# Kernel optimization log

Measured on AMD Instinct MI355X. Metric: run time of the kernel, lower is better.

Reference implementation:

```python
import jax, jax.numpy as jnp
import numpy as np

D = 1024
H = 4
HD = D // H
B = 256
L = 64
DILATIONS = (1, 4, 8, 16)


def setup_inputs() -> dict:
    key = jax.random.key(0)
    ks = jax.random.split(key, 12)
    s = 1.0 / np.sqrt(D)
    return {
        "x": jax.random.normal(ks[0], (B, D), jnp.float32),
        "hist": jax.random.normal(ks[1], (L, B, D), jnp.float32),
        "Wq": jax.random.normal(ks[2], (D, D), jnp.float32) * s,
        "bq": jnp.zeros((D,), jnp.float32),
        "Wk": jax.random.normal(ks[3], (D, D), jnp.float32) * s,
        "bk": jnp.zeros((D,), jnp.float32),
        "Wv": jax.random.normal(ks[4], (D, D), jnp.float32) * s,
        "bv": jnp.zeros((D,), jnp.float32),
        "Wo": jax.random.normal(ks[5], (D, D), jnp.float32) * s,
        "bo": jnp.zeros((D,), jnp.float32),
        "dil_w": jnp.full((len(DILATIONS),), 1.0 / len(DILATIONS), jnp.float32),
        "gamma": jnp.ones((D,), jnp.float32),
        "beta": jnp.zeros((D,), jnp.float32),
    }


def reference(x, hist, Wq, bq, Wk, bk, Wv, bv, Wo, bo, dil_w, gamma, beta):
    scale = 1.0 / np.sqrt(HD)
    q = (x @ Wq + bq).reshape(B, H, HD)  # (B, H, HD)
    attended = []
    for d in DILATIONS:
        # history frames at stride d, concatenated along dim 0 (faithful to torch.cat)
        frames = hist[::d].reshape(-1, D)              # (T', D), T' = ceil(L/d)*B
        k = (frames @ Wk + bk).reshape(-1, H, HD)      # (T', H, HD)
        v = (frames @ Wv + bv).reshape(-1, H, HD)
        s = jnp.einsum('bhd,thd->bht', q, k) * scale   # (B, H, T')
        a = jax.nn.softmax(s, axis=-1)
        attended.append(jnp.einsum('bht,thd->bhd', a, v).reshape(B, D))
    w = jax.nn.softmax(dil_w, axis=0)
    combined = sum(w[i] * attended[i] for i in range(len(DILATIONS)))
    y = x + combined @ Wo + bo
    mu = jnp.mean(y, axis=-1, keepdims=True)
    var = jnp.var(y, axis=-1, keepdims=True)
    return (y - mu) / jnp.sqrt(var + 1e-5) * gamma + beta
```

## Files before the change

### kernel.cpp

```cpp
#include <hip/hip_runtime.h>


#define DD    1024
#define TALL  16384

typedef _Float16 half8  __attribute__((ext_vector_type(8)));
typedef _Float16 half4v __attribute__((ext_vector_type(4)));
typedef float    floatx4 __attribute__((ext_vector_type(4)));
typedef unsigned int u32;

static const size_t OFF_WQT = 0;
static const size_t OFF_WKT = 2097152;
static const size_t OFF_WVT = 4194304;
static const size_t OFF_WOT = 6291456;
static const size_t OFF_XB  = 8388608;
static const size_t OFF_QS  = 8912896;
static const size_t OFF_HB  = 16777216;
static const size_t OFF_S   = OFF_HB;
static const size_t OFF_KB  = 50331648;
static const size_t OFF_PVP = OFF_KB;
static const size_t OFF_VT  = 83886080;
static const size_t OFF_OPP = 117440512;
static const size_t OFF_CB  = 134483968;

__device__ __forceinline__ void gl_lds16(const void* g, void* l) {
  __builtin_amdgcn_global_load_lds((const __attribute__((address_space(1))) u32*)g,
                                   (__attribute__((address_space(3))) u32*)l, 16, 0, 0);
}

__global__ void wtrans_kernel(const float* __restrict__ W0, const float* __restrict__ W1,
                              const float* __restrict__ W2, const float* __restrict__ W3,
                              _Float16* __restrict__ T0, _Float16* __restrict__ T1,
                              _Float16* __restrict__ T2, _Float16* __restrict__ T3) {
  const float* W; _Float16* T;
  switch (blockIdx.z) {
    case 0: W = W0; T = T0; break;
    case 1: W = W1; T = T1; break;
    case 2: W = W2; T = T2; break;
    default: W = W3; T = T3; break;
  }
  __shared__ float tile[32][33];
  int tx = threadIdx.x & 31, ty = threadIdx.x >> 5;
  int k0 = blockIdx.x * 32, n0 = blockIdx.y * 32;
#pragma unroll
  for (int i = 0; i < 4; i++) {
    int r = ty + i * 8;
    tile[r][tx] = W[(size_t)(k0 + r) * DD + n0 + tx];
  }
  __syncthreads();
#pragma unroll
  for (int i = 0; i < 4; i++) {
    int r = ty + i * 8;
    T[(size_t)(n0 + r) * DD + k0 + tx] = (_Float16)tile[tx][r];
  }
}

__global__ void cvt2_kernel(const float* __restrict__ a, _Float16* __restrict__ oa, int na4,
                            const float* __restrict__ b, _Float16* __restrict__ ob, int nb4) {
  int i = blockIdx.x * 256 + threadIdx.x;
  const float* src; _Float16* dst;
  if (i < na4) { src = a; dst = oa; }
  else { i -= na4; if (i >= nb4) return; src = b; dst = ob; }
  float4 v = ((const float4*)src)[i];
  half4v h = {(_Float16)v.x, (_Float16)v.y, (_Float16)v.z, (_Float16)v.w};
  *(half4v*)(dst + 4 * (size_t)i) = h;
}

__device__ __forceinline__ void gemm_core(const _Float16* __restrict__ A, size_t lda,
                                          const _Float16* __restrict__ B, size_t ldb,
                                          int kIters, _Float16* As, _Float16* Bs,
                                          int tid, floatx4 acc[4][4]) {
  int lane = tid & 63, w = tid >> 6;
  int l15 = lane & 15, quad = lane >> 4;
  int wm = (w >> 1) * 64, wn = (w & 1) * 64;
  int swz = ((tid & 3) ^ ((tid >> 3) & 3)) * 8;
  int pch = (quad ^ ((l15 >> 1) & 3)) * 8;
  const char* gA0 = (const char*)(A + (size_t)(tid >> 2) * lda + swz);
  const char* gA1 = (const char*)(A + ((size_t)(tid >> 2) + 64) * lda + swz);
  const char* gB0 = (const char*)(B + (size_t)(tid >> 2) * ldb + swz);
  const char* gB1 = (const char*)(B + ((size_t)(tid >> 2) + 64) * ldb + swz);
  _Float16* lA0 = As + w * 512; _Float16* lA1 = As + 2048 + w * 512;
  _Float16* lB0 = Bs + w * 512; _Float16* lB1 = Bs + 2048 + w * 512;
  for (int kk = 0; kk < kIters; kk++) {
    __syncthreads();
    size_t off = (size_t)kk * 64;
    gl_lds16(gA0 + off, lA0);
    gl_lds16(gA1 + off, lA1);
    gl_lds16(gB0 + off, lB0);
    gl_lds16(gB1 + off, lB1);
    __syncthreads();
    half8 a[4];
#pragma unroll
    for (int mi = 0; mi < 4; mi++) a[mi] = *(const half8*)&As[(wm + mi * 16 + l15) * 32 + pch];
#pragma unroll
    for (int ni = 0; ni < 4; ni++) {
      half8 b8 = *(const half8*)&Bs[(wn + ni * 16 + l15) * 32 + pch];
#pragma unroll
      for (int mi = 0; mi < 4; mi++)
        acc[mi][ni] = __builtin_amdgcn_mfma_f32_16x16x32_f16(a[mi], b8, acc[mi][ni], 0, 0, 0);
    }
  }
}

template <bool OUTF32>
__launch_bounds__(256, 3)
__global__ void gemm_f16_kernel(const _Float16* __restrict__ A, size_t lda, size_t aoffz,
                                const _Float16* __restrict__ B, size_t ldb, size_t boffz,
                                int kIters, const float* __restrict__ bias, float scale,
                                void* __restrict__ C, size_t ldc, size_t coffz) {
  __shared__ __align__(16) _Float16 As[4096];
  __shared__ __align__(16) _Float16 Bs[4096];
  int tid = threadIdx.x;
  const _Float16* Ab = A + aoffz * blockIdx.z + (size_t)(blockIdx.y * 128) * lda;
  const _Float16* Bb = B + boffz * blockIdx.z + (size_t)(blockIdx.x * 128) * ldb;
  floatx4 acc[4][4];
  floatx4 zero = {0.f, 0.f, 0.f, 0.f};
#pragma unroll
  for (int a = 0; a < 4; a++)
#pragma unroll
    for (int b = 0; b < 4; b++) acc[a][b] = zero;
  gemm_core(Ab, lda, Bb, ldb, kIters, As, Bs, tid, acc);
  int lane = tid & 63, w = tid >> 6;
  int l15 = lane & 15, quad = lane >> 4;
  int wm = (w >> 1) * 64, wn = (w & 1) * 64;
#pragma unroll
  for (int mi = 0; mi < 4; mi++)
#pragma unroll
    for (int ni = 0; ni < 4; ni++) {
      int colg = blockIdx.x * 128 + wn + ni * 16 + l15;
      float bv = bias ? bias[colg] : 0.f;
#pragma unroll
      for (int r = 0; r < 4; r++) {
        int rowg = blockIdx.y * 128 + wm + mi * 16 + quad * 4 + r;
        float v = (acc[mi][ni][r] + bv) * scale;
        size_t idx = coffz * blockIdx.z + (size_t)rowg * ldc + colg;
        if (OUTF32) ((float*)C)[idx] = v;
        else ((_Float16*)C)[idx] = (_Float16)v;
      }
    }
}

__launch_bounds__(256, 2)
__global__ void gemm_kv_kernel(const _Float16* __restrict__ A,
                               const _Float16* __restrict__ WkT, const _Float16* __restrict__ WvT,
                               const float* __restrict__ bk, const float* __restrict__ bv,
                               _Float16* __restrict__ K, _Float16* __restrict__ Vt) {
  __shared__ __align__(16) _Float16 As[4096];
  __shared__ __align__(16) _Float16 Bk[4096];
  __shared__ __align__(16) _Float16 Bv[4096];
  int tid = threadIdx.x;
  int lane = tid & 63, w = tid >> 6;
  int l15 = lane & 15, quad = lane >> 4;
  int wm = (w >> 1) * 64, wn = (w & 1) * 64;
  int m0 = blockIdx.y * 128, n0 = blockIdx.x * 128;
  int swz = ((tid & 3) ^ ((tid >> 3) & 3)) * 8;
  int pch = (quad ^ ((l15 >> 1) & 3)) * 8;
  floatx4 accK[4][4], accV[4][4];
  floatx4 zero = {0.f, 0.f, 0.f, 0.f};
#pragma unroll
  for (int a = 0; a < 4; a++)
#pragma unroll
    for (int b = 0; b < 4; b++) { accK[a][b] = zero; accV[a][b] = zero; }
  const char* gA0 = (const char*)(A + ((size_t)m0 + (tid >> 2)) * 1024 + swz);
  const char* gA1 = gA0 + 64 * 1024 * 2;
  const char* gK0 = (const char*)(WkT + ((size_t)n0 + (tid >> 2)) * 1024 + swz);
  const char* gK1 = gK0 + 64 * 1024 * 2;
  const char* gV0 = (const char*)(WvT + ((size_t)n0 + (tid >> 2)) * 1024 + swz);
  const char* gV1 = gV0 + 64 * 1024 * 2;
  _Float16* lA0 = As + w * 512; _Float16* lA1 = As + 2048 + w * 512;
  _Float16* lK0 = Bk + w * 512; _Float16* lK1 = Bk + 2048 + w * 512;
  _Float16* lV0 = Bv + w * 512; _Float16* lV1 = Bv + 2048 + w * 512;
  for (int kk = 0; kk < 32; kk++) {
    __syncthreads();
    size_t off = (size_t)kk * 64;
    gl_lds16(gA0 + off, lA0); gl_lds16(gA1 + off, lA1);
    gl_lds16(gK0 + off, lK0); gl_lds16(gK1 + off, lK1);
    gl_lds16(gV0 + off, lV0); gl_lds16(gV1 + off, lV1);
    __syncthreads();
    half8 a[4];
#pragma unroll
    for (int mi = 0; mi < 4; mi++) a[mi] = *(const half8*)&As[(wm + mi * 16 + l15) * 32 + pch];
#pragma unroll
    for (int ni = 0; ni < 4; ni++) {
      half8 k8 = *(const half8*)&Bk[(wn + ni * 16 + l15) * 32 + pch];
      half8 v8 = *(const half8*)&Bv[(wn + ni * 16 + l15) * 32 + pch];
#pragma unroll
      for (int mi = 0; mi < 4; mi++) {
        accK[mi][ni] = __builtin_amdgcn_mfma_f32_16x16x32_f16(a[mi], k8, accK[mi][ni], 0, 0, 0);
        accV[mi][ni] = __builtin_amdgcn_mfma_f32_16x16x32_f16(a[mi], v8, accV[mi][ni], 0, 0, 0);
      }
    }
  }
#pragma unroll
  for (int mi = 0; mi < 4; mi++)
#pragma unroll
    for (int ni = 0; ni < 4; ni++) {
      int col = n0 + wn + ni * 16 + l15;
      float bkv = bk[col], bvv = bv[col];
      int row0 = m0 + wm + mi * 16 + quad * 4;
#pragma unroll
      for (int r = 0; r < 4; r++)
        K[(size_t)(row0 + r) * 1024 + col] = (_Float16)(accK[mi][ni][r] + bkv);
      half4v vv = {(_Float16)(accV[mi][ni][0] + bvv), (_Float16)(accV[mi][ni][1] + bvv),
                   (_Float16)(accV[mi][ni][2] + bvv), (_Float16)(accV[mi][ni][3] + bvv)};
      *(half4v*)&Vt[(size_t)col * TALL + row0] = vv;
    }
}

__global__ void softmax_kernel(_Float16* __restrict__ S, const float* __restrict__ dil_w) {
  int r = blockIdx.x, tid = threadIdx.x;
  _Float16* row = S + (size_t)r * TALL;
  int lane = tid & 63, w = tid >> 6;
  half8 v[8];
  float mloc = -1e30f;
#pragma unroll
  for (int i = 0; i < 8; i++) {
    v[i] = *(const half8*)&row[((size_t)i * 256 + tid) * 8];
#pragma unroll
    for (int j = 0; j < 8; j++) mloc = fmaxf(mloc, (float)v[i][j]);
  }
  __shared__ float wmax[4];
  __shared__ float Zf[64];
  __shared__ float Zd[4];
  __shared__ float cf[64];
#pragma unroll
  for (int off = 1; off <= 32; off <<= 1) mloc = fmaxf(mloc, __shfl_xor(mloc, off, 64));
  if (lane == 0) wmax[w] = mloc;
  __syncthreads();
  float m = fmaxf(fmaxf(wmax[0], wmax[1]), fmaxf(wmax[2], wmax[3]));
  float es[8];
#pragma unroll
  for (int i = 0; i < 8; i++) {
    float s = 0.f;
#pragma unroll
    for (int j = 0; j < 8; j++) s += __expf((float)v[i][j] - m);
#pragma unroll
    for (int off = 1; off <= 16; off <<= 1) s += __shfl_xor(s, off, 64);
    es[i] = s;
  }
  if ((lane & 31) == 0) {
    int half = tid >> 5;
#pragma unroll
    for (int i = 0; i < 8; i++) Zf[i * 8 + half] = es[i];
  }
  __syncthreads();
  if (tid < 4) {
    int step = 1 << (tid + (tid ? 1 : 0));
    float z = 0.f;
    for (int f = 0; f < 64; f += step) z += Zf[f];
    Zd[tid] = z;
  }
  __syncthreads();
  if (tid < 64) {
    float w0 = dil_w[0], w1 = dil_w[1], w2 = dil_w[2], w3 = dil_w[3];
    float wmx = fmaxf(fmaxf(w0, w1), fmaxf(w2, w3));
    float e0 = __expf(w0 - wmx), e1 = __expf(w1 - wmx), e2 = __expf(w2 - wmx), e3 = __expf(w3 - wmx);
    float wsum = e0 + e1 + e2 + e3;
    float c = (e0 / wsum) / Zd[0];
    if ((tid & 3) == 0) c += (e1 / wsum) / Zd[1];
    if ((tid & 7) == 0) c += (e2 / wsum) / Zd[2];
    if ((tid & 15) == 0) c += (e3 / wsum) / Zd[3];
    cf[tid] = c * 256.0f;
  }
  __syncthreads();
#pragma unroll
  for (int i = 0; i < 8; i++) {
    float c = cf[i * 8 + (tid >> 5)];
    half8 o;
#pragma unroll
    for (int j = 0; j < 8; j++) o[j] = (_Float16)(__expf((float)v[i][j] - m) * c);
    *(half8*)&row[((size_t)i * 256 + tid) * 8] = o;
  }
}

__launch_bounds__(256, 3)
__global__ void gemm_pv_kernel(const _Float16* __restrict__ P, const _Float16* __restrict__ Vt,
                               float* __restrict__ part) {
  __shared__ __align__(16) _Float16 As[4096];
  __shared__ __align__(16) _Float16 Bs[4096];
  int tid = threadIdx.x;
  int h = blockIdx.z >> 5, sp = blockIdx.z & 31;
  const _Float16* Ab = P + (size_t)h * 4194304 + (size_t)(blockIdx.y * 128) * TALL + sp * 512;
  const _Float16* Bb = Vt + (size_t)(h * 256 + blockIdx.x * 128) * TALL + sp * 512;
  floatx4 acc[4][4];
  floatx4 zero = {0.f, 0.f, 0.f, 0.f};
#pragma unroll
  for (int a = 0; a < 4; a++)
#pragma unroll
    for (int b = 0; b < 4; b++) acc[a][b] = zero;
  gemm_core(Ab, TALL, Bb, TALL, 16, As, Bs, tid, acc);
  int lane = tid & 63, w = tid >> 6;
  int l15 = lane & 15, quad = lane >> 4;
  int wm = (w >> 1) * 64, wn = (w & 1) * 64;
#pragma unroll
  for (int mi = 0; mi < 4; mi++)
#pragma unroll
    for (int ni = 0; ni < 4; ni++) {
      int featg = h * 256 + blockIdx.x * 128 + wn + ni * 16 + l15;
#pragma unroll
      for (int r = 0; r < 4; r++) {
        int q = blockIdx.y * 128 + wm + mi * 16 + quad * 4 + r;
        part[((size_t)(sp * 256 + q)) * 1024 + featg] = acc[mi][ni][r];
      }
    }
}

__global__ void reduce_kernel(const float* __restrict__ part, _Float16* __restrict__ comb) {
  int q = blockIdx.x;
  int f4 = threadIdx.x * 4;
  float4 s = {0.f, 0.f, 0.f, 0.f};
  for (int sp = 0; sp < 32; sp++) {
    float4 p = *(const float4*)&part[((size_t)(sp * 256 + q)) * 1024 + f4];
    s.x += p.x; s.y += p.y; s.z += p.z; s.w += p.w;
  }
  const float inv = 1.f / 256.f;
  half4v o = {(_Float16)(s.x * inv), (_Float16)(s.y * inv), (_Float16)(s.z * inv), (_Float16)(s.w * inv)};
  *(half4v*)&comb[(size_t)q * 1024 + f4] = o;
}

__global__ void ln_kernel(const float* __restrict__ x, const float* __restrict__ part2,
                          const float* __restrict__ bo, const float* __restrict__ gamma,
                          const float* __restrict__ beta, float* __restrict__ out) {
  int b = blockIdx.x, t = threadIdx.x;
  __shared__ float red[8];
  float y[4];
  float sum = 0.f, sq = 0.f;
#pragma unroll
  for (int i = 0; i < 4; i++) {
    int j = t + i * 256;
    float v = x[(size_t)b * 1024 + j] + bo[j];
#pragma unroll
    for (int z = 0; z < 4; z++) v += part2[(size_t)z * 262144 + (size_t)b * 1024 + j];
    y[i] = v;
    sum += v;
    sq += v * v;
  }
#pragma unroll
  for (int off = 1; off < 64; off <<= 1) {
    sum += __shfl_xor(sum, off, 64);
    sq += __shfl_xor(sq, off, 64);
  }
  int w = t >> 6, lane = t & 63;
  if (lane == 0) { red[w] = sum; red[4 + w] = sq; }
  __syncthreads();
  sum = red[0] + red[1] + red[2] + red[3];
  sq = red[4] + red[5] + red[6] + red[7];
  float mu = sum * (1.f / 1024.f);
  float var = sq * (1.f / 1024.f) - mu * mu;
  float inv = rsqrtf(var + 1e-5f);
#pragma unroll
  for (int i = 0; i < 4; i++) {
    int j = t + i * 256;
    out[(size_t)b * 1024 + j] = (y[i] - mu) * inv * gamma[j] + beta[j];
  }
}

extern "C" void kernel_launch(void* const* d_in, const int* in_sizes, int n_in,
                              void* d_out, int out_size, void* d_ws, size_t ws_size,
                              hipStream_t stream) {
  const float* x     = (const float*)d_in[0];
  const float* hist  = (const float*)d_in[1];
  const float* Wq    = (const float*)d_in[2];
  const float* bq    = (const float*)d_in[3];
  const float* Wk    = (const float*)d_in[4];
  const float* bk    = (const float*)d_in[5];
  const float* Wv    = (const float*)d_in[6];
  const float* bv    = (const float*)d_in[7];
  const float* Wo    = (const float*)d_in[8];
  const float* bo    = (const float*)d_in[9];
  const float* dil_w = (const float*)d_in[10];
  const float* gamma = (const float*)d_in[11];
  const float* beta  = (const float*)d_in[12];
  char* ws = (char*)d_ws;

  _Float16* WqT   = (_Float16*)(ws + OFF_WQT);
  _Float16* WkT   = (_Float16*)(ws + OFF_WKT);
  _Float16* WvT   = (_Float16*)(ws + OFF_WVT);
  _Float16* WoT   = (_Float16*)(ws + OFF_WOT);
  _Float16* xb    = (_Float16*)(ws + OFF_XB);
  _Float16* Qs    = (_Float16*)(ws + OFF_QS);
  _Float16* histb = (_Float16*)(ws + OFF_HB);
  _Float16* Sb    = (_Float16*)(ws + OFF_S);
  _Float16* Kb    = (_Float16*)(ws + OFF_KB);
  _Float16* Vtb   = (_Float16*)(ws + OFF_VT);
  float* pvpart   = (float*)(ws + OFF_PVP);
  float* oppart   = (float*)(ws + OFF_OPP);
  _Float16* comb  = (_Float16*)(ws + OFF_CB);

  wtrans_kernel<<<dim3(32, 32, 4), 256, 0, stream>>>(Wq, Wk, Wv, Wo, WqT, WkT, WvT, WoT);
  cvt2_kernel<<<dim3(16640), 256, 0, stream>>>(hist, histb, 4194304, x, xb, 65536);
  gemm_f16_kernel<false><<<dim3(8, 2, 1), 256, 0, stream>>>(
      xb, 1024, 0, WqT, 1024, 0, 32, bq, 0.0625f, (void*)Qs, 1024, 0);
  gemm_kv_kernel<<<dim3(8, 128), 256, 0, stream>>>(histb, WkT, WvT, bk, bv, Kb, Vtb);
  gemm_f16_kernel<false><<<dim3(128, 2, 4), 256, 0, stream>>>(
      Qs, 1024, 256, Kb, 1024, 256, 8, nullptr, 1.0f, (void*)Sb, TALL, 4194304);
  softmax_kernel<<<dim3(1024), 256, 0, stream>>>(Sb, dil_w);
  gemm_pv_kernel<<<dim3(2, 2, 128), 256, 0, stream>>>(Sb, Vtb, pvpart);
  reduce_kernel<<<dim3(256), 256, 0, stream>>>(pvpart, comb);
  gemm_f16_kernel<true><<<dim3(8, 2, 4), 256, 0, stream>>>(
      comb, 1024, 256, WoT, 1024, 256, 8, nullptr, 1.0f, (void*)oppart, 1024, 262144);
  ln_kernel<<<dim3(256), 256, 0, stream>>>(x, oppart, bo, gamma, beta, (float*)d_out);
}
```

Before: 327.4 us.

## Reassociate attention to avoid computing K and V projections over history

Rather than projecting all 16384 history frames through Wk and Wv, the query is folded into Wk per head (G = Q·Wk_h^T) so scores come straight from G·hist^T. Likewise P·hist is computed first, then multiplied by a precomputed fused Wv·Wo per head. The bv·Wo term is added in the layernorm kernel, and bk is dropped because it shifts every score in a row equally. This removes the large KV GEMM and its stores, but adds a transposed fp16 copy of hist, a P·hist GEMM with a 4096-wide per-head output, and a split-K partial reduction.

```diff
diff --git a/kernel.cpp b/kernel.cpp
--- a/kernel.cpp
+++ b/kernel.cpp
@@ -9,61 +9,94 @@
 typedef float    floatx4 __attribute__((ext_vector_type(4)));
 typedef unsigned int u32;
 
-static const size_t OFF_WQT = 0;
-static const size_t OFF_WKT = 2097152;
-static const size_t OFF_WVT = 4194304;
-static const size_t OFF_WOT = 6291456;
-static const size_t OFF_XB  = 8388608;
-static const size_t OFF_QS  = 8912896;
-static const size_t OFF_HB  = 16777216;
-static const size_t OFF_S   = OFF_HB;
-static const size_t OFF_KB  = 50331648;
-static const size_t OFF_PVP = OFF_KB;
-static const size_t OFF_VT  = 83886080;
-static const size_t OFF_OPP = 117440512;
-static const size_t OFF_CB  = 134483968;
+static const size_t OFF_WQT  = 0;
+static const size_t OFF_WOT  = 2097152;
+static const size_t OFF_WV16 = 4194304;
+static const size_t OFF_WK16 = 6291456;
+static const size_t OFF_XB   = 8388608;
+static const size_t OFF_QS   = 8912896;
+static const size_t OFF_G    = 9437184;
+static const size_t OFF_WVOT = 11534336;
+static const size_t OFF_BVWO = 19922944;
+static const size_t OFF_OPP  = 19988480;
+static const size_t OFF_PHR  = 24182784;
+static const size_t OFF_HB   = 33554432;
+static const size_t OFF_PHP  = OFF_HB;
+static const size_t OFF_HT   = 67108864;
+static const size_t OFF_S    = 100663296;
 
 __device__ __forceinline__ void gl_lds16(const void* g, void* l) {
   __builtin_amdgcn_global_load_lds((const __attribute__((address_space(1))) u32*)g,
                                    (__attribute__((address_space(3))) u32*)l, 16, 0, 0);
 }
 
-__global__ void wtrans_kernel(const float* __restrict__ W0, const float* __restrict__ W1,
-                              const float* __restrict__ W2, const float* __restrict__ W3,
-                              _Float16* __restrict__ T0, _Float16* __restrict__ T1,
-                              _Float16* __restrict__ T2, _Float16* __restrict__ T3) {
-  const float* W; _Float16* T;
-  switch (blockIdx.z) {
-    case 0: W = W0; T = T0; break;
-    case 1: W = W1; T = T1; break;
-    case 2: W = W2; T = T2; break;
-    default: W = W3; T = T3; break;
-  }
-  __shared__ float tile[32][33];
-  int tx = threadIdx.x & 31, ty = threadIdx.x >> 5;
-  int k0 = blockIdx.x * 32, n0 = blockIdx.y * 32;
-#pragma unroll
-  for (int i = 0; i < 4; i++) {
-    int r = ty + i * 8;
-    tile[r][tx] = W[(size_t)(k0 + r) * DD + n0 + tx];
-  }
-  __syncthreads();
-#pragma unroll
-  for (int i = 0; i < 4; i++) {
-    int r = ty + i * 8;
-    T[(size_t)(n0 + r) * DD + k0 + tx] = (_Float16)tile[tx][r];
-  }
-}
-
-__global__ void cvt2_kernel(const float* __restrict__ a, _Float16* __restrict__ oa, int na4,
-                            const float* __restrict__ b, _Float16* __restrict__ ob, int nb4) {
-  int i = blockIdx.x * 256 + threadIdx.x;
-  const float* src; _Float16* dst;
-  if (i < na4) { src = a; dst = oa; }
-  else { i -= na4; if (i >= nb4) return; src = b; dst = ob; }
-  float4 v = ((const float4*)src)[i];
-  half4v h = {(_Float16)v.x, (_Float16)v.y, (_Float16)v.z, (_Float16)v.w};
-  *(half4v*)(dst + 4 * (size_t)i) = h;
+__global__ void prep_kernel(const float* __restrict__ Wq, const float* __restrict__ Wo,
+                            const float* __restrict__ Wv, const float* __restrict__ Wk,
+                            const float* __restrict__ hist, const float* __restrict__ x,
+                            _Float16* __restrict__ WqT, _Float16* __restrict__ WoT,
+                            _Float16* __restrict__ Wv16, _Float16* __restrict__ Wk16,
+                            _Float16* __restrict__ histb, _Float16* __restrict__ histT,
+                            _Float16* __restrict__ xb) {
+  int bid = blockIdx.x, tid = threadIdx.x;
+  if (bid < 2048) {
+    const float* W = (bid < 1024) ? Wq : Wo;
+    _Float16* T = (bid < 1024) ? WqT : WoT;
+    int tile = bid & 1023;
+    int k0 = (tile & 31) * 32, n0 = (tile >> 5) * 32;
+    __shared__ float t32[32][33];
+    int tx = tid & 31, ty = tid >> 5;
+#pragma unroll
+    for (int i = 0; i < 4; i++) {
+      int r = ty + i * 8;
+      t32[r][tx] = W[(size_t)(k0 + r) * DD + n0 + tx];
+    }
+    __syncthreads();
+#pragma unroll
+    for (int i = 0; i < 4; i++) {
+      int r = ty + i * 8;
+      T[(size_t)(n0 + r) * DD + k0 + tx] = (_Float16)t32[tx][r];
+    }
+  } else if (bid < 20736) {
+    const float* src; _Float16* dst; size_t i;
+    if (bid < 3072)       { src = Wv;   dst = Wv16;  i = (size_t)(bid - 2048) * 256 + tid; }
+    else if (bid < 4096)  { src = Wk;   dst = Wk16;  i = (size_t)(bid - 3072) * 256 + tid; }
+    else if (bid < 20480) { src = hist; dst = histb; i = (size_t)(bid - 4096) * 256 + tid; }
+    else                  { src = x;    dst = xb;    i = (size_t)(bid - 20480) * 256 + tid; }
+    float4 v = ((const float4*)src)[i];
+    half4v h = {(_Float16)v.x, (_Float16)v.y, (_Float16)v.z, (_Float16)v.w};
+    *(half4v*)(dst + 4 * i) = h;
+  } else {
+    int tb = bid - 20736;
+    int t0 = (tb & 255) * 64, f0 = (tb >> 8) * 64;
+    __shared__ _Float16 lt[64][72];
+    int r = tid >> 2, c0 = (tid & 3) * 16;
+#pragma unroll
+    for (int i = 0; i < 4; i++) {
+      float4 v = *(const float4*)&hist[(size_t)(t0 + r) * 1024 + f0 + c0 + i * 4];
+      half4v h = {(_Float16)v.x, (_Float16)v.y, (_Float16)v.z, (_Float16)v.w};
+      *(half4v*)&lt[r][c0 + i * 4] = h;
+    }
+    __syncthreads();
+    int fr = tid >> 2, tc0 = (tid & 3) * 16;
+    half8 o0, o1;
+#pragma unroll
+    for (int j = 0; j < 8; j++) { o0[j] = lt[tc0 + j][fr]; o1[j] = lt[tc0 + 8 + j][fr]; }
+    *(half8*)&histT[(size_t)(f0 + fr) * TALL + t0 + tc0] = o0;
+    *(half8*)&histT[(size_t)(f0 + fr) * TALL + t0 + tc0 + 8] = o1;
+  }
+}
+
+__global__ void bvwo_kernel(const float* __restrict__ bv, const _Float16* __restrict__ WoT,
+                            float* __restrict__ bvwo) {
+  int j = blockIdx.x * 256 + threadIdx.x;
+  const half8* row = (const half8*)(WoT + (size_t)j * 1024);
+  float acc = 0.f;
+  for (int c = 0; c < 128; c++) {
+    half8 w = row[c];
+#pragma unroll
+    for (int e = 0; e < 8; e++) acc += bv[c * 8 + e] * (float)w[e];
+  }
+  bvwo[j] = acc;
 }
 
 __device__ __forceinline__ void gemm_core(const _Float16* __restrict__ A, size_t lda,
@@ -140,71 +173,51 @@
     }
 }
 
-__launch_bounds__(256, 2)
-__global__ void gemm_kv_kernel(const _Float16* __restrict__ A,
-                               const _Float16* __restrict__ WkT, const _Float16* __restrict__ WvT,
-                               const float* __restrict__ bk, const float* __restrict__ bv,
-                               _Float16* __restrict__ K, _Float16* __restrict__ Vt) {
+__launch_bounds__(256, 3)
+__global__ void gemm_ph_kernel(const _Float16* __restrict__ P, const _Float16* __restrict__ histT,
+                               float* __restrict__ part) {
   __shared__ __align__(16) _Float16 As[4096];
-  __shared__ __align__(16) _Float16 Bk[4096];
-  __shared__ __align__(16) _Float16 Bv[4096];
+  __shared__ __align__(16) _Float16 Bs[4096];
   int tid = threadIdx.x;
+  int h = blockIdx.z >> 3, sp = blockIdx.z & 7;
+  const _Float16* Ab = P + (size_t)h * 4194304 + (size_t)(blockIdx.y * 128) * TALL + sp * 2048;
+  const _Float16* Bb = histT + (size_t)(blockIdx.x * 128) * TALL + sp * 2048;
+  floatx4 acc[4][4];
+  floatx4 zero = {0.f, 0.f, 0.f, 0.f};
+#pragma unroll
+  for (int a = 0; a < 4; a++)
+#pragma unroll
+    for (int b = 0; b < 4; b++) acc[a][b] = zero;
+  gemm_core(Ab, TALL, Bb, TALL, 64, As, Bs, tid, acc);
   int lane = tid & 63, w = tid >> 6;
   int l15 = lane & 15, quad = lane >> 4;
   int wm = (w >> 1) * 64, wn = (w & 1) * 64;
-  int m0 = blockIdx.y * 128, n0 = blockIdx.x * 128;
-  int swz = ((tid & 3) ^ ((tid >> 3) & 3)) * 8;
-  int pch = (quad ^ ((l15 >> 1) & 3)) * 8;
-  floatx4 accK[4][4], accV[4][4];
-  floatx4 zero = {0.f, 0.f, 0.f, 0.f};
-#pragma unroll
-  for (int a = 0; a < 4; a++)
-#pragma unroll
-    for (int b = 0; b < 4; b++) { accK[a][b] = zero; accV[a][b] = zero; }
-  const char* gA0 = (const char*)(A + ((size_t)m0 + (tid >> 2)) * 1024 + swz);
-  const char* gA1 = gA0 + 64 * 1024 * 2;
-  const char* gK0 = (const char*)(WkT + ((size_t)n0 + (tid >> 2)) * 1024 + swz);
-  const char* gK1 = gK0 + 64 * 1024 * 2;
-  const char* gV0 = (const char*)(WvT + ((size_t)n0 + (tid >> 2)) * 1024 + swz);
-  const char* gV1 = gV0 + 64 * 1024 * 2;
-  _Float16* lA0 = As + w * 512; _Float16* lA1 = As + 2048 + w * 512;
-  _Float16* lK0 = Bk + w * 512; _Float16* lK1 = Bk + 2048 + w * 512;
-  _Float16* lV0 = Bv + w * 512; _Float16* lV1 = Bv + 2048 + w * 512;
-  for (int kk = 0; kk < 32; kk++) {
-    __syncthreads();
-    size_t off = (size_t)kk * 64;
-    gl_lds16(gA0 + off, lA0); gl_lds16(gA1 + off, lA1);
-    gl_lds16(gK0 + off, lK0); gl_lds16(gK1 + off, lK1);
-    gl_lds16(gV0 + off, lV0); gl_lds16(gV1 + off, lV1);
-    __syncthreads();
-    half8 a[4];
-#pragma unroll
-    for (int mi = 0; mi < 4; mi++) a[mi] = *(const half8*)&As[(wm + mi * 16 + l15) * 32 + pch];
+#pragma unroll
+  for (int mi = 0; mi < 4; mi++)
 #pragma unroll
     for (int ni = 0; ni < 4; ni++) {
-      half8 k8 = *(const half8*)&Bk[(wn + ni * 16 + l15) * 32 + pch];
-      half8 v8 = *(const half8*)&Bv[(wn + ni * 16 + l15) * 32 + pch];
-#pragma unroll
-      for (int mi = 0; mi < 4; mi++) {
-        accK[mi][ni] = __builtin_amdgcn_mfma_f32_16x16x32_f16(a[mi], k8, accK[mi][ni], 0, 0, 0);
-        accV[mi][ni] = __builtin_amdgcn_mfma_f32_16x16x32_f16(a[mi], v8, accV[mi][ni], 0, 0, 0);
+      int k = blockIdx.x * 128 + wn + ni * 16 + l15;
+#pragma unroll
+      for (int r = 0; r < 4; r++) {
+        int q = blockIdx.y * 128 + wm + mi * 16 + quad * 4 + r;
+        part[(size_t)blockIdx.z * 262144 + (size_t)q * 1024 + k] = acc[mi][ni][r];
       }
     }
-  }
-#pragma unroll
-  for (int mi = 0; mi < 4; mi++)
-#pragma unroll
-    for (int ni = 0; ni < 4; ni++) {
-      int col = n0 + wn + ni * 16 + l15;
-      float bkv = bk[col], bvv = bv[col];
-      int row0 = m0 + wm + mi * 16 + quad * 4;
-#pragma unroll
-      for (int r = 0; r < 4; r++)
-        K[(size_t)(row0 + r) * 1024 + col] = (_Float16)(accK[mi][ni][r] + bkv);
-      half4v vv = {(_Float16)(accV[mi][ni][0] + bvv), (_Float16)(accV[mi][ni][1] + bvv),
-                   (_Float16)(accV[mi][ni][2] + bvv), (_Float16)(accV[mi][ni][3] + bvv)};
-      *(half4v*)&Vt[(size_t)col * TALL + row0] = vv;
-    }
+}
+
+__global__ void reduce_ph_kernel(const float* __restrict__ part, _Float16* __restrict__ PHred) {
+  size_t e4 = ((size_t)blockIdx.x * 256 + threadIdx.x) * 4;
+  int q = (int)(e4 >> 12);
+  int hk = (int)(e4 & 4095);
+  int h = hk >> 10, k = hk & 1023;
+  float4 s = {0.f, 0.f, 0.f, 0.f};
+#pragma unroll
+  for (int sp = 0; sp < 8; sp++) {
+    float4 p = *(const float4*)&part[(size_t)(h * 8 + sp) * 262144 + (size_t)q * 1024 + k];
+    s.x += p.x; s.y += p.y; s.z += p.z; s.w += p.w;
+  }
+  half4v o = {(_Float16)s.x, (_Float16)s.y, (_Float16)s.z, (_Float16)s.w};
+  *(half4v*)&PHred[e4] = o;
 }
 
 __global__ void softmax_kernel(_Float16* __restrict__ S, const float* __restrict__ dil_w) {
@@ -273,54 +286,10 @@
   }
 }
 
-__launch_bounds__(256, 3)
-__global__ void gemm_pv_kernel(const _Float16* __restrict__ P, const _Float16* __restrict__ Vt,
-                               float* __restrict__ part) {
-  __shared__ __align__(16) _Float16 As[4096];
-  __shared__ __align__(16) _Float16 Bs[4096];
-  int tid = threadIdx.x;
-  int h = blockIdx.z >> 5, sp = blockIdx.z & 31;
-  const _Float16* Ab = P + (size_t)h * 4194304 + (size_t)(blockIdx.y * 128) * TALL + sp * 512;
-  const _Float16* Bb = Vt + (size_t)(h * 256 + blockIdx.x * 128) * TALL + sp * 512;
-  floatx4 acc[4][4];
-  floatx4 zero = {0.f, 0.f, 0.f, 0.f};
-#pragma unroll
-  for (int a = 0; a < 4; a++)
-#pragma unroll
-    for (int b = 0; b < 4; b++) acc[a][b] = zero;
-  gemm_core(Ab, TALL, Bb, TALL, 16, As, Bs, tid, acc);
-  int lane = tid & 63, w = tid >> 6;
-  int l15 = lane & 15, quad = lane >> 4;
-  int wm = (w >> 1) * 64, wn = (w & 1) * 64;
-#pragma unroll
-  for (int mi = 0; mi < 4; mi++)
-#pragma unroll
-    for (int ni = 0; ni < 4; ni++) {
-      int featg = h * 256 + blockIdx.x * 128 + wn + ni * 16 + l15;
-#pragma unroll
-      for (int r = 0; r < 4; r++) {
-        int q = blockIdx.y * 128 + wm + mi * 16 + quad * 4 + r;
-        part[((size_t)(sp * 256 + q)) * 1024 + featg] = acc[mi][ni][r];
-      }
-    }
-}
-
-__global__ void reduce_kernel(const float* __restrict__ part, _Float16* __restrict__ comb) {
-  int q = blockIdx.x;
-  int f4 = threadIdx.x * 4;
-  float4 s = {0.f, 0.f, 0.f, 0.f};
-  for (int sp = 0; sp < 32; sp++) {
-    float4 p = *(const float4*)&part[((size_t)(sp * 256 + q)) * 1024 + f4];
-    s.x += p.x; s.y += p.y; s.z += p.z; s.w += p.w;
-  }
-  const float inv = 1.f / 256.f;
-  half4v o = {(_Float16)(s.x * inv), (_Float16)(s.y * inv), (_Float16)(s.z * inv), (_Float16)(s.w * inv)};
-  *(half4v*)&comb[(size_t)q * 1024 + f4] = o;
-}
-
 __global__ void ln_kernel(const float* __restrict__ x, const float* __restrict__ part2,
-                          const float* __restrict__ bo, const float* __restrict__ gamma,
-                          const float* __restrict__ beta, float* __restrict__ out) {
+                          const float* __restrict__ bo, const float* __restrict__ bvwo,
+                          const float* __restrict__ gamma, const float* __restrict__ beta,
+                          float* __restrict__ out) {
   int b = blockIdx.x, t = threadIdx.x;
   __shared__ float red[8];
   float y[4];
@@ -328,7 +297,7 @@
 #pragma unroll
   for (int i = 0; i < 4; i++) {
     int j = t + i * 256;
-    float v = x[(size_t)b * 1024 + j] + bo[j];
+    float v = x[(size_t)b * 1024 + j] + bo[j] + bvwo[j];
 #pragma unroll
     for (int z = 0; z < 4; z++) v += part2[(size_t)z * 262144 + (size_t)b * 1024 + j];
     y[i] = v;
@@ -363,7 +332,6 @@
   const float* Wq    = (const float*)d_in[2];
   const float* bq    = (const float*)d_in[3];
   const float* Wk    = (const float*)d_in[4];
-  const float* bk    = (const float*)d_in[5];
   const float* Wv    = (const float*)d_in[6];
   const float* bv    = (const float*)d_in[7];
   const float* Wo    = (const float*)d_in[8];
@@ -374,30 +342,37 @@
   char* ws = (char*)d_ws;
 
   _Float16* WqT   = (_Float16*)(ws + OFF_WQT);
-  _Float16* WkT   = (_Float16*)(ws + OFF_WKT);
-  _Float16* WvT   = (_Float16*)(ws + OFF_WVT);
   _Float16* WoT   = (_Float16*)(ws + OFF_WOT);
+  _Float16* Wv16  = (_Float16*)(ws + OFF_WV16);
+  _Float16* Wk16  = (_Float16*)(ws + OFF_WK16);
   _Float16* xb    = (_Float16*)(ws + OFF_XB);
   _Float16* Qs    = (_Float16*)(ws + OFF_QS);
+  _Float16* G     = (_Float16*)(ws + OFF_G);
+  _Float16* WVOT  = (_Float16*)(ws + OFF_WVOT);
+  float* bvwo     = (float*)(ws + OFF_BVWO);
+  float* oppart   = (float*)(ws + OFF_OPP);
+  _Float16* PHred = (_Float16*)(ws + OFF_PHR);
   _Float16* histb = (_Float16*)(ws + OFF_HB);
+  float* phpart   = (float*)(ws + OFF_PHP);
+  _Float16* histT = (_Float16*)(ws + OFF_HT);
   _Float16* Sb    = (_Float16*)(ws + OFF_S);
-  _Float16* Kb    = (_Float16*)(ws + OFF_KB);
-  _Float16* Vtb   = (_Float16*)(ws + OFF_VT);
-  float* pvpart   = (float*)(ws + OFF_PVP);
-  float* oppart   = (float*)(ws + OFF_OPP);
-  _Float16* comb  = (_Float16*)(ws + OFF_CB);
-
-  wtrans_kernel<<<dim3(32, 32, 4), 256, 0, stream>>>(Wq, Wk, Wv, Wo, WqT, WkT, WvT, WoT);
-  cvt2_kernel<<<dim3(16640), 256, 0, stream>>>(hist, histb, 4194304, x, xb, 65536);
+
+  prep_kernel<<<dim3(24832), 256, 0, stream>>>(Wq, Wo, Wv, Wk, hist, x,
+                                               WqT, WoT, Wv16, Wk16, histb, histT, xb);
+  bvwo_kernel<<<dim3(4), 256, 0, stream>>>(bv, WoT, bvwo);
+  gemm_f16_kernel<false><<<dim3(8, 8, 4), 256, 0, stream>>>(
+      WoT, 1024, 256, Wv16, 1024, 256, 8, nullptr, 1.0f, (void*)WVOT, 4096, 1024);
   gemm_f16_kernel<false><<<dim3(8, 2, 1), 256, 0, stream>>>(
       xb, 1024, 0, WqT, 1024, 0, 32, bq, 0.0625f, (void*)Qs, 1024, 0);
-  gemm_kv_kernel<<<dim3(8, 128), 256, 0, stream>>>(histb, WkT, WvT, bk, bv, Kb, Vtb);
+  gemm_f16_kernel<false><<<dim3(8, 2, 4), 256, 0, stream>>>(
+      Qs, 1024, 256, Wk16, 1024, 256, 8, nullptr, 1.0f, (void*)G, 1024, 262144);
   gemm_f16_kernel<false><<<dim3(128, 2, 4), 256, 0, stream>>>(
-      Qs, 1024, 256, Kb, 1024, 256, 8, nullptr, 1.0f, (void*)Sb, TALL, 4194304);
+      G, 1024, 262144, histb, 1024, 0, 32, nullptr, 1.0f, (void*)Sb, TALL, 4194304);
   softmax_kernel<<<dim3(1024), 256, 0, stream>>>(Sb, dil_w);
-  gemm_pv_kernel<<<dim3(2, 2, 128), 256, 0, stream>>>(Sb, Vtb, pvpart);
-  reduce_kernel<<<dim3(256), 256, 0, stream>>>(pvpart, comb);
+  gemm_ph_kernel<<<dim3(8, 2, 32), 256, 0, stream>>>(Sb, histT, phpart);
+  reduce_ph_kernel<<<dim3(1024), 256, 0, stream>>>(phpart, PHred);
   gemm_f16_kernel<true><<<dim3(8, 2, 4), 256, 0, stream>>>(
-      comb, 1024, 256, WoT, 1024, 256, 8, nullptr, 1.0f, (void*)oppart, 1024, 262144);
-  ln_kernel<<<dim3(256), 256, 0, stream>>>(x, oppart, bo, gamma, beta, (float*)d_out);
-}
+      PHred, 4096, 1024, WVOT, 4096, 1024, 32, nullptr, 1.0f / 256.0f,
+      (void*)oppart, 1024, 262144);
+  ln_kernel<<<dim3(256), 256, 0, stream>>>(x, oppart, bo, bvwo, gamma, beta, (float*)d_out);
+}
```

Result: slower. 360.4 us (+10.1%).
